# Optimization experiments

Hardware: AMD Instinct MI355X
Metric: run time of the kernel (lower is better)

The kernel has to match this reference:

```python
import jax, jax.numpy as jnp
import numpy as np

DIM_IN = 1024
DIM_OUT = 1024
B = 8192


def setup_inputs() -> dict:
    key = jax.random.key(0)
    ks = jax.random.split(key, 8)
    d = DIM_IN + DIM_OUT
    bound = 1.0 / np.sqrt(d)
    def lin(kw, kb):
        W = jax.random.uniform(kw, (d, DIM_OUT), jnp.float32, -bound, bound)
        b = jax.random.uniform(kb, (DIM_OUT,), jnp.float32, -bound, bound)
        return W, b
    kx, kh, kc, kp = ks[0], ks[1], ks[2], ks[3]
    pw = jax.random.split(kp, 8)
    W_I, b_I = lin(pw[0], pw[1])
    W_F, b_F = lin(pw[2], pw[3])
    W_G, b_G = lin(pw[4], pw[5])
    W_O, b_O = lin(pw[6], pw[7])
    return {
        "x": jax.random.normal(kx, (B, DIM_IN), jnp.float32),
        "h": jax.random.normal(kh, (B, DIM_OUT), jnp.float32),
        "c": jax.random.normal(kc, (B, DIM_OUT), jnp.float32),
        "W_I": W_I, "b_I": b_I,
        "W_F": W_F, "b_F": b_F,
        "W_G": W_G, "b_G": b_G,
        "W_O": W_O, "b_O": b_O,
    }


def reference(x, h, c, W_I, b_I, W_F, b_F, W_G, b_G, W_O, b_O):
    X = jnp.concatenate([x, h], axis=-1)  # [B, dimIn+dimOut]
    # Fuse the 4 gate projections into one GEMM: [B,d] @ [d, 4*dimOut]
    W = jnp.concatenate([W_I, W_F, W_G, W_O], axis=1)
    b = jnp.concatenate([b_I, b_F, b_G, b_O], axis=0)
    gates = X @ W + b
    i_, f_, g_, o_ = jnp.split(gates, 4, axis=-1)
    I = jax.nn.sigmoid(i_)
    F = jax.nn.sigmoid(f_)
    G = jnp.tanh(g_)
    O = jax.nn.sigmoid(o_)
    C = F * c + I * G
    return O * jnp.tanh(C), C
```

## Files before the change

### kernel.cpp

```cpp
#include <hip/hip_runtime.h>
#include <cstdint>


#define B_ROWS 8192
#define DK 2048
#define DOUT 1024
#define TM 128
#define TN 128
#define BK 64

typedef __bf16 bf16x8 __attribute__((ext_vector_type(8)));
typedef __bf16 bf16x4 __attribute__((ext_vector_type(4)));
typedef float f32x4 __attribute__((ext_vector_type(4)));

__device__ inline void load16_to_lds(const __bf16* gsrc, __bf16* ldst) {
    __builtin_amdgcn_global_load_lds(
        (const __attribute__((address_space(1))) void*)gsrc,
        (__attribute__((address_space(3))) void*)ldst,
        16, 0, 0);
}

__device__ inline float fast_sigmoid(float x) {
    return __builtin_amdgcn_rcpf(1.0f + __builtin_amdgcn_exp2f(-1.442695041f * x));
}
__device__ inline float fast_tanh(float x) {
    return 1.0f - 2.0f * __builtin_amdgcn_rcpf(1.0f + __builtin_amdgcn_exp2f(2.885390082f * x));
}

__global__ __launch_bounds__(256) void prep_x(const float* __restrict__ x,
                                              const float* __restrict__ h,
                                              __bf16* __restrict__ X) {
    int id = blockIdx.x * 256 + threadIdx.x;
    int b = id >> 8;
    int k = (id & 255) * 8;
    const float* src = (k < 1024) ? &x[(size_t)b * 1024 + k]
                                  : &h[(size_t)b * 1024 + (k - 1024)];
    float4 v0 = *(const float4*)src;
    float4 v1 = *(const float4*)(src + 4);
    bf16x8 o = { (__bf16)v0.x, (__bf16)v0.y, (__bf16)v0.z, (__bf16)v0.w,
                 (__bf16)v1.x, (__bf16)v1.y, (__bf16)v1.z, (__bf16)v1.w };
    *(bf16x8*)&X[(size_t)b * 2048 + k] = o;
}

__global__ __launch_bounds__(256) void prep_w(const float* __restrict__ WI,
                                              const float* __restrict__ WF,
                                              const float* __restrict__ WG,
                                              const float* __restrict__ WO,
                                              __bf16* __restrict__ Wt) {
    int kb = blockIdx.x;
    int jb = blockIdx.y;
    int j0 = jb * 32;
    __shared__ float t[64][33];
    int tx = threadIdx.x, ty = threadIdx.y;
    int idx = ty * 32 + tx;
    const float* Ws[4] = {WI, WF, WG, WO};
#pragma unroll
    for (int g = 0; g < 4; ++g) {
        const float* W = Ws[g];
#pragma unroll
        for (int yy = 0; yy < 64; yy += 8) {
            int k = kb * 64 + ty + yy;
            t[ty + yy][tx] = W[(size_t)k * 1024 + j0 + tx];
        }
        __syncthreads();
#pragma unroll
        for (int w = 0; w < 2; ++w) {
            int slot = w * 256 + idx;
            int r = slot >> 4;
            int k0 = (slot & 15) * 4;
            bf16x4 o = { (__bf16)t[k0 + 0][r], (__bf16)t[k0 + 1][r],
                         (__bf16)t[k0 + 2][r], (__bf16)t[k0 + 3][r] };
            int npp = (jb * 2 + (r >> 4)) * 64 + g * 16 + (r & 15);
            *(bf16x4*)&Wt[(size_t)npp * 2048 + kb * 64 + k0] = o;
        }
        __syncthreads();
    }
}

__global__ __launch_bounds__(256) void lstm_gemm(
    const __bf16* __restrict__ Xbf, const __bf16* __restrict__ Wt,
    const float* __restrict__ c,
    const float* __restrict__ bI, const float* __restrict__ bF,
    const float* __restrict__ bG, const float* __restrict__ bO,
    float* __restrict__ outH, float* __restrict__ outC)
{
    __shared__ __bf16 As[TM * BK];
    __shared__ __bf16 Bs[TN * BK];

    const int t = threadIdx.x;
    const int lane = t & 63;
    const int wave = t >> 6;
    const int wm = wave >> 1;
    const int wn = wave & 1;
    const int m0 = blockIdx.x * TM;
    const int nb = blockIdx.y;
    const int n0 = nb * TN;

    f32x4 acc[4][4];
#pragma unroll
    for (int i = 0; i < 4; ++i)
#pragma unroll
        for (int j = 0; j < 4; ++j) acc[i][j] = (f32x4){0.f, 0.f, 0.f, 0.f};

    const int rs = t >> 3;
    const int kc = (t & 7) * 8;
    const __bf16* gA = Xbf + (size_t)(m0 + rs) * DK + kc;
    const __bf16* gB = Wt + (size_t)(n0 + rs) * DK + kc;
    __bf16* lA = As + wave * 512;
    __bf16* lB = Bs + wave * 512;

    const int lr = lane & 15;
    const int kh = (lane >> 4) * 8;
    const int arow = wm * 64 + lr;
    const int brow = wn * 64 + lr;

    for (int kk = 0; kk < DK / BK; ++kk) {
#pragma unroll
        for (int q = 0; q < 4; ++q) {
            load16_to_lds(gA + (size_t)(q * 32) * DK, lA + q * 2048);
            load16_to_lds(gB + (size_t)(q * 32) * DK, lB + q * 2048);
        }
        gA += BK; gB += BK;
        __syncthreads();

#pragma unroll
        for (int ks = 0; ks < BK; ks += 32) {
            bf16x8 a[4], b[4];
#pragma unroll
            for (int i = 0; i < 4; ++i)
                a[i] = *(const bf16x8*)&As[(arow + i * 16) * BK + ks + kh];
#pragma unroll
            for (int j = 0; j < 4; ++j)
                b[j] = *(const bf16x8*)&Bs[(brow + j * 16) * BK + ks + kh];
#pragma unroll
            for (int i = 0; i < 4; ++i)
#pragma unroll
                for (int j = 0; j < 4; ++j)
                    acc[i][j] = __builtin_amdgcn_mfma_f32_16x16x32_bf16(a[i], b[j], acc[i][j], 0, 0, 0);
        }
        __syncthreads();
    }

    const int col = lane & 15;
    const int j = (nb * 2 + wn) * 16 + col;
    const float biI = bI[j], biF = bF[j], biG = bG[j], biO = bO[j];
    const int rbase = m0 + wm * 64 + (lane >> 4) * 4;
#pragma unroll
    for (int i = 0; i < 4; ++i) {
#pragma unroll
        for (int r = 0; r < 4; ++r) {
            int row = rbase + i * 16 + r;
            float I = fast_sigmoid(acc[i][0][r] + biI);
            float F = fast_sigmoid(acc[i][1][r] + biF);
            float G = fast_tanh(acc[i][2][r] + biG);
            float O = fast_sigmoid(acc[i][3][r] + biO);
            size_t idx = (size_t)row * DOUT + j;
            float Cn = F * c[idx] + I * G;
            outH[idx] = O * fast_tanh(Cn);
            outC[idx] = Cn;
        }
    }
}

extern "C" void kernel_launch(void* const* d_in, const int* in_sizes, int n_in,
                              void* d_out, int out_size, void* d_ws, size_t ws_size,
                              hipStream_t stream) {
    const float* x  = (const float*)d_in[0];
    const float* h  = (const float*)d_in[1];
    const float* c  = (const float*)d_in[2];
    const float* WI = (const float*)d_in[3];
    const float* bI = (const float*)d_in[4];
    const float* WF = (const float*)d_in[5];
    const float* bF = (const float*)d_in[6];
    const float* WG = (const float*)d_in[7];
    const float* bG = (const float*)d_in[8];
    const float* WO = (const float*)d_in[9];
    const float* bO = (const float*)d_in[10];

    __bf16* Xbf = (__bf16*)d_ws;
    __bf16* Wt  = (__bf16*)((char*)d_ws + (size_t)B_ROWS * DK * 2);
    float* outH = (float*)d_out;
    float* outC = outH + (size_t)B_ROWS * DOUT;

    prep_x<<<(B_ROWS * DK / 8) / 256, 256, 0, stream>>>(x, h, Xbf);
    prep_w<<<dim3(DK / 64, DOUT / 32), dim3(32, 8), 0, stream>>>(WI, WF, WG, WO, Wt);
    lstm_gemm<<<dim3(B_ROWS / TM, 4 * DOUT / TN), 256, 0, stream>>>(
        Xbf, Wt, c, bI, bF, bG, bO, outH, outC);
}
```

Measured before the change: 367.8 us.

## Double-buffer GEMM LDS tiles with BK=32 and merge prep kernels

The GEMM main loop now uses two LDS buffers with a K-step of 32. The next tile's global-to-LDS loads are issued before the MFMAs on the current tile, and one barrier per iteration replaces two. This is meant to overlap memory latency with compute. The x/h and weight conversion kernels are also merged into a single launch to save one kernel launch. Halving BK doubles the number of loop iterations and barriers. There is also a possible race: the only thing ordering the async LDS loads against their consumers is the barrier placed before the next issue.

```diff
diff --git a/kernel.cpp b/kernel.cpp
--- a/kernel.cpp
+++ b/kernel.cpp
@@ -7,7 +7,7 @@
 #define DOUT 1024
 #define TM 128
 #define TN 128
-#define BK 64
+#define BK 32
 
 typedef __bf16 bf16x8 __attribute__((ext_vector_type(8)));
 typedef __bf16 bf16x4 __attribute__((ext_vector_type(4)));
@@ -27,53 +27,54 @@
     return 1.0f - 2.0f * __builtin_amdgcn_rcpf(1.0f + __builtin_amdgcn_exp2f(2.885390082f * x));
 }
 
-__global__ __launch_bounds__(256) void prep_x(const float* __restrict__ x,
-                                              const float* __restrict__ h,
-                                              __bf16* __restrict__ X) {
-    int id = blockIdx.x * 256 + threadIdx.x;
-    int b = id >> 8;
-    int k = (id & 255) * 8;
-    const float* src = (k < 1024) ? &x[(size_t)b * 1024 + k]
-                                  : &h[(size_t)b * 1024 + (k - 1024)];
-    float4 v0 = *(const float4*)src;
-    float4 v1 = *(const float4*)(src + 4);
-    bf16x8 o = { (__bf16)v0.x, (__bf16)v0.y, (__bf16)v0.z, (__bf16)v0.w,
-                 (__bf16)v1.x, (__bf16)v1.y, (__bf16)v1.z, (__bf16)v1.w };
-    *(bf16x8*)&X[(size_t)b * 2048 + k] = o;
-}
-
-__global__ __launch_bounds__(256) void prep_w(const float* __restrict__ WI,
-                                              const float* __restrict__ WF,
-                                              const float* __restrict__ WG,
-                                              const float* __restrict__ WO,
-                                              __bf16* __restrict__ Wt) {
-    int kb = blockIdx.x;
-    int jb = blockIdx.y;
-    int j0 = jb * 32;
-    __shared__ float t[64][33];
-    int tx = threadIdx.x, ty = threadIdx.y;
-    int idx = ty * 32 + tx;
-    const float* Ws[4] = {WI, WF, WG, WO};
+__global__ __launch_bounds__(256) void prep_all(
+    const float* __restrict__ x, const float* __restrict__ h,
+    const float* __restrict__ WI, const float* __restrict__ WF,
+    const float* __restrict__ WG, const float* __restrict__ WO,
+    __bf16* __restrict__ X, __bf16* __restrict__ Wt)
+{
+    __shared__ float tile[64][33];
+    int bid = blockIdx.x;
+    int t = threadIdx.x;
+    if (bid < 8192) {
+        int id = bid * 256 + t;
+        int b = id >> 8;
+        int k = (id & 255) * 8;
+        const float* src = (k < 1024) ? &x[(size_t)b * 1024 + k]
+                                      : &h[(size_t)b * 1024 + (k - 1024)];
+        float4 v0 = *(const float4*)src;
+        float4 v1 = *(const float4*)(src + 4);
+        bf16x8 o = { (__bf16)v0.x, (__bf16)v0.y, (__bf16)v0.z, (__bf16)v0.w,
+                     (__bf16)v1.x, (__bf16)v1.y, (__bf16)v1.z, (__bf16)v1.w };
+        *(bf16x8*)&X[(size_t)b * 2048 + k] = o;
+    } else {
+        int wb = bid - 8192;
+        int kb = wb >> 5;
+        int jb = wb & 31;
+        int j0 = jb * 32;
+        int tx = t & 31, ty = t >> 5;
+        const float* Ws[4] = {WI, WF, WG, WO};
 #pragma unroll
-    for (int g = 0; g < 4; ++g) {
-        const float* W = Ws[g];
+        for (int g = 0; g < 4; ++g) {
+            const float* W = Ws[g];
 #pragma unroll
-        for (int yy = 0; yy < 64; yy += 8) {
-            int k = kb * 64 + ty + yy;
-            t[ty + yy][tx] = W[(size_t)k * 1024 + j0 + tx];
+            for (int yy = 0; yy < 64; yy += 8) {
+                int k = kb * 64 + ty + yy;
+                tile[ty + yy][tx] = W[(size_t)k * 1024 + j0 + tx];
+            }
+            __syncthreads();
+#pragma unroll
+            for (int w = 0; w < 2; ++w) {
+                int slot = w * 256 + t;
+                int r = slot >> 4;
+                int k0 = (slot & 15) * 4;
+                bf16x4 o = { (__bf16)tile[k0 + 0][r], (__bf16)tile[k0 + 1][r],
+                             (__bf16)tile[k0 + 2][r], (__bf16)tile[k0 + 3][r] };
+                int npp = (jb * 2 + (r >> 4)) * 64 + g * 16 + (r & 15);
+                *(bf16x4*)&Wt[(size_t)npp * 2048 + kb * 64 + k0] = o;
+            }
+            __syncthreads();
         }
-        __syncthreads();
-#pragma unroll
-        for (int w = 0; w < 2; ++w) {
-            int slot = w * 256 + idx;
-            int r = slot >> 4;
-            int k0 = (slot & 15) * 4;
-            bf16x4 o = { (__bf16)t[k0 + 0][r], (__bf16)t[k0 + 1][r],
-                         (__bf16)t[k0 + 2][r], (__bf16)t[k0 + 3][r] };
-            int npp = (jb * 2 + (r >> 4)) * 64 + g * 16 + (r & 15);
-            *(bf16x4*)&Wt[(size_t)npp * 2048 + kb * 64 + k0] = o;
-        }
-        __syncthreads();
     }
 }
 
@@ -84,8 +85,8 @@
     const float* __restrict__ bG, const float* __restrict__ bO,
     float* __restrict__ outH, float* __restrict__ outC)
 {
-    __shared__ __bf16 As[TM * BK];
-    __shared__ __bf16 Bs[TN * BK];
+    __shared__ __bf16 As[2][TM * BK];
+    __shared__ __bf16 Bs[2][TN * BK];
 
     const int t = threadIdx.x;
     const int lane = t & 63;
@@ -102,43 +103,48 @@
 #pragma unroll
         for (int j = 0; j < 4; ++j) acc[i][j] = (f32x4){0.f, 0.f, 0.f, 0.f};
 
-    const int rs = t >> 3;
-    const int kc = (t & 7) * 8;
-    const __bf16* gA = Xbf + (size_t)(m0 + rs) * DK + kc;
-    const __bf16* gB = Wt + (size_t)(n0 + rs) * DK + kc;
-    __bf16* lA = As + wave * 512;
-    __bf16* lB = Bs + wave * 512;
+    const int r0 = t >> 2, kc0 = (t & 3) * 8;
+    const __bf16* gA0 = Xbf + (size_t)(m0 + r0) * DK + kc0;
+    const __bf16* gA1 = Xbf + (size_t)(m0 + 64 + r0) * DK + kc0;
+    const __bf16* gB0 = Wt + (size_t)(n0 + r0) * DK + kc0;
+    const __bf16* gB1 = Wt + (size_t)(n0 + 64 + r0) * DK + kc0;
+    const int l0 = wave * 512;
+    const int l1 = 2048 + wave * 512;
 
     const int lr = lane & 15;
     const int kh = (lane >> 4) * 8;
     const int arow = wm * 64 + lr;
     const int brow = wn * 64 + lr;
 
+    load16_to_lds(gA0, &As[0][l0]);
+    load16_to_lds(gA1, &As[0][l1]);
+    load16_to_lds(gB0, &Bs[0][l0]);
+    load16_to_lds(gB1, &Bs[0][l1]);
+    gA0 += BK; gA1 += BK; gB0 += BK; gB1 += BK;
+
     for (int kk = 0; kk < DK / BK; ++kk) {
+        __syncthreads();
+        if (kk < DK / BK - 1) {
+            const int nb2 = (kk + 1) & 1;
+            load16_to_lds(gA0, &As[nb2][l0]);
+            load16_to_lds(gA1, &As[nb2][l1]);
+            load16_to_lds(gB0, &Bs[nb2][l0]);
+            load16_to_lds(gB1, &Bs[nb2][l1]);
+            gA0 += BK; gA1 += BK; gB0 += BK; gB1 += BK;
+        }
+        const int cb = kk & 1;
+        bf16x8 a[4], b[4];
 #pragma unroll
-        for (int q = 0; q < 4; ++q) {
-            load16_to_lds(gA + (size_t)(q * 32) * DK, lA + q * 2048);
-            load16_to_lds(gB + (size_t)(q * 32) * DK, lB + q * 2048);
-        }
-        gA += BK; gB += BK;
-        __syncthreads();
-
+        for (int i = 0; i < 4; ++i)
+            a[i] = *(const bf16x8*)&As[cb][(arow + i * 16) * BK + kh];
 #pragma unroll
-        for (int ks = 0; ks < BK; ks += 32) {
-            bf16x8 a[4], b[4];
+        for (int j = 0; j < 4; ++j)
+            b[j] = *(const bf16x8*)&Bs[cb][(brow + j * 16) * BK + kh];
 #pragma unroll
-            for (int i = 0; i < 4; ++i)
-                a[i] = *(const bf16x8*)&As[(arow + i * 16) * BK + ks + kh];
+        for (int i = 0; i < 4; ++i)
 #pragma unroll
             for (int j = 0; j < 4; ++j)
-                b[j] = *(const bf16x8*)&Bs[(brow + j * 16) * BK + ks + kh];
-#pragma unroll
-            for (int i = 0; i < 4; ++i)
-#pragma unroll
-                for (int j = 0; j < 4; ++j)
-                    acc[i][j] = __builtin_amdgcn_mfma_f32_16x16x32_bf16(a[i], b[j], acc[i][j], 0, 0, 0);
-        }
-        __syncthreads();
+                acc[i][j] = __builtin_amdgcn_mfma_f32_16x16x32_bf16(a[i], b[j], acc[i][j], 0, 0, 0);
     }
 
     const int col = lane & 15;
@@ -182,8 +188,7 @@
     float* outH = (float*)d_out;
     float* outC = outH + (size_t)B_ROWS * DOUT;
 
-    prep_x<<<(B_ROWS * DK / 8) / 256, 256, 0, stream>>>(x, h, Xbf);
-    prep_w<<<dim3(DK / 64, DOUT / 32), dim3(32, 8), 0, stream>>>(WI, WF, WG, WO, Wt);
+    prep_all<<<8192 + 1024, 256, 0, stream>>>(x, h, WI, WF, WG, WO, Xbf, Wt);
     lstm_gemm<<<dim3(B_ROWS / TM, 4 * DOUT / TN), 256, 0, stream>>>(
         Xbf, Wt, c, bI, bF, bG, bO, outH, outC);
 }
```

New measurement: 394.5 us. 7.3% more time.
